# Kernel optimization log

Measured on AMD Instinct MI355X. Metric: run time of the kernel, lower is better.

Reference implementation:

```python
import jax, jax.numpy as jnp
import numpy as np
from jax import lax

N = 32768      # total nodes (8 graphs x 4096)
E = 262144     # edges (avg degree 8)
B = 8          # graphs in batch
TW = 25        # time window
H = 128        # hidden features
L = 6          # GNN layers
NV = 1         # n_variables (pos_t only)
SD = 1         # spatial dim
TMAX, TMIN, RES_T = 4.0, 0.0, 250.0
BD_LOW, BD_UP = 0.0, 16.0
EPS = 1e-5


def swish(x):
    return x * jax.nn.sigmoid(x)


def setup_inputs() -> dict:
    key = jax.random.key(0)
    ks = jax.random.split(key, 32)
    s = 0.05
    u = jax.random.normal(ks[0], (N, TW), jnp.float32)
    pos_t = jax.random.uniform(ks[1], (N, 1), jnp.float32) * TMAX
    pos_x = jax.random.uniform(ks[2], (N, 1), jnp.float32) * BD_UP
    pos = jnp.concatenate([pos_t, pos_x], axis=-1)
    edge_index = jax.random.randint(ks[3], (2, E), 0, N, jnp.int64)
    batch = jnp.repeat(jnp.arange(B, dtype=jnp.int64), N // B)
    d_in = TW + SD + NV          # 27
    d_msg = 2 * H + TW + SD + NV  # 282
    d_upd = H + H + NV            # 257
    We1 = jax.random.normal(ks[4], (d_in, H), jnp.float32) * s
    be1 = jnp.zeros((H,), jnp.float32)
    We2 = jax.random.normal(ks[5], (H, H), jnp.float32) * s
    be2 = jnp.zeros((H,), jnp.float32)
    Wm1 = jax.random.normal(ks[6], (L, d_msg, H), jnp.float32) * s
    bm1 = jnp.zeros((L, H), jnp.float32)
    Wm2 = jax.random.normal(ks[7], (L, H, H), jnp.float32) * s
    bm2 = jnp.zeros((L, H), jnp.float32)
    Wu1 = jax.random.normal(ks[8], (L, d_upd, H), jnp.float32) * s
    bu1 = jnp.zeros((L, H), jnp.float32)
    Wu2 = jax.random.normal(ks[9], (L, H, H), jnp.float32) * s
    bu2 = jnp.zeros((L, H), jnp.float32)
    Wc1 = jax.random.normal(ks[10], (8, 1, 16), jnp.float32) * s  # OIH
    bc1 = jnp.zeros((8,), jnp.float32)
    Wc2 = jax.random.normal(ks[11], (1, 8, 14), jnp.float32) * s
    bc2 = jnp.zeros((1,), jnp.float32)
    return dict(u=u, pos=pos, edge_index=edge_index, batch=batch,
                We1=We1, be1=be1, We2=We2, be2=be2,
                Wm1=Wm1, bm1=bm1, Wm2=Wm2, bm2=bm2,
                Wu1=Wu1, bu1=bu1, Wu2=Wu2, bu2=bu2,
                Wc1=Wc1, bc1=bc1, Wc2=Wc2, bc2=bc2)


def _mpnn(u, pos, edge_index, batch, We1, be1, We2, be2,
          Wm1, bm1, Wm2, bm2, Wu1, bu1, Wu2, bu2, Wc1, bc1, Wc2, bc2):
    src = edge_index[0]   # j (source)
    tgt = edge_index[1]   # i (target)
    pos_t = pos[:, 0:1] / TMAX
    pos_x = (pos[:, 1:] - BD_LOW) / (BD_UP - BD_LOW)
    variables = pos_t  # eq_variables empty -> only normalized time

    node_input = jnp.concatenate([u, pos_x, variables], axis=-1)  # [N, 27]
    h = swish(node_input @ We1 + be1)
    h = swish(h @ We2 + be2)

    # in-degree for scatter-mean (empty targets -> 0 like PyG mean)
    cnt = jnp.zeros((N,), jnp.float32).at[tgt].add(1.0)
    cnt = jnp.maximum(cnt, 1.0)[:, None]
    # per-graph node counts for InstanceNorm
    gcnt = jax.ops.segment_sum(jnp.ones((N,), jnp.float32), batch, num_segments=B)[:, None]

    u_diff_e = u[tgt] - u[src]          # [E, TW]
    p_diff_e = pos_x[tgt] - pos_x[src]  # [E, SD]
    var_i_e = variables[tgt]            # [E, NV]

    for l in range(L):
        # message: gather -> MLP per edge
        m_in = jnp.concatenate([h[tgt], h[src], u_diff_e, p_diff_e, var_i_e], axis=-1)  # [E, 282]
        msg = swish(m_in @ Wm1[l] + bm1[l])
        msg = swish(msg @ Wm2[l] + bm2[l])
        # scatter-mean aggregate onto targets
        agg = jax.ops.segment_sum(msg, tgt, num_segments=N) / cnt  # [N, H]
        # node update MLP, residual (in_features == out_features)
        up = jnp.concatenate([h, agg, variables], axis=-1)  # [N, 257]
        up = swish(up @ Wu1[l] + bu1[l])
        up = swish(up @ Wu2[l] + bu2[l])
        h = h + up
        # InstanceNorm per graph (no affine), biased variance
        mean = jax.ops.segment_sum(h, batch, num_segments=B) / gcnt      # [B, H]
        sq = jax.ops.segment_sum(h * h, batch, num_segments=B) / gcnt    # [B, H]
        var = sq - mean * mean
        h = (h - mean[batch]) / jnp.sqrt(var[batch] + EPS)

    # output CNN: tw=25 branch
    hc = h[:, None, :]  # [N, 1, 128]
    dn = ('NCH', 'OIH', 'NCH')
    c = lax.conv_general_dilated(hc, Wc1, (3,), 'VALID', dimension_numbers=dn) + bc1[None, :, None]
    c = swish(c)
    c = lax.conv_general_dilated(c, Wc2, (1,), 'VALID', dimension_numbers=dn) + bc2[None, :, None]
    diff = c[:, 0, :]  # [N, 25]

    dt = (TMAX - TMIN) / RES_T
    dt_cum = jnp.arange(1, TW + 1, dtype=jnp.float32) * dt  # cumsum of ones*dt
    out = u[:, -1:] + dt_cum[None, :] * diff
    return out


def reference(u, pos, edge_index, batch, We1, be1, We2, be2,
              Wm1, bm1, Wm2, bm2, Wu1, bu1, Wu2, bu2, Wc1, bc1, Wc2, bc2):
    return _mpnn(u, pos, edge_index, batch, We1, be1, We2, be2,
                 Wm1, bm1, Wm2, bm2, Wu1, bu1, Wu2, bu2, Wc1, bc1, Wc2, bc2)
```

## Files before the change

### kernel.cpp

```cpp
#include <hip/hip_runtime.h>
#include <stdint.h>

#define N_NODES 32768
#define N_EDGES 262144
#define NB 8
#define TW 25

typedef __attribute__((ext_vector_type(8))) short short8;
typedef __attribute__((ext_vector_type(4))) float floatx4;

#if defined(__has_builtin)
#if __has_builtin(__builtin_amdgcn_cvt_pk_bf16_f32)
#define HAVE_CVT_PK_BF16 1
#endif
#endif

__device__ __forceinline__ float swishf(float x) {
    return x * __builtin_amdgcn_rcpf(1.0f + __expf(-x));
}

__device__ __forceinline__ unsigned short f2bf(float x) {
    union { float f; unsigned u; } v; v.f = x;
    unsigned r = v.u + 0x7FFFu + ((v.u >> 16) & 1u);
    return (unsigned short)(r >> 16);
}
__device__ __forceinline__ unsigned pkbf(float a, float b) {
#ifdef HAVE_CVT_PK_BF16
    typedef __attribute__((ext_vector_type(2))) __bf16 bf16x2;
    union { bf16x2 v; unsigned u; } cv;
    cv.v = __builtin_amdgcn_cvt_pk_bf16_f32(a, b);
    return cv.u;
#else
    return (unsigned)f2bf(a) | ((unsigned)f2bf(b) << 16);
#endif
}
__device__ __forceinline__ float bf2f(unsigned short b) {
    union { unsigned u; float f; } v; v.u = ((unsigned)b) << 16; return v.f;
}

__global__ void init_kernel(const float* __restrict__ pos,
                            float* __restrict__ posx, float* __restrict__ post) {
    int i = blockIdx.x * 256 + threadIdx.x;
    if (i < N_NODES) {
        post[i] = pos[i * 2 + 0] * 0.25f;
        posx[i] = pos[i * 2 + 1] * 0.0625f;
    }
}

__global__ void deg_kernel(const int* __restrict__ tgt, int* __restrict__ deg) {
    int i = blockIdx.x * 256 + threadIdx.x;
    if (i < N_EDGES) atomicAdd(&deg[tgt[i]], 1);
}

__global__ __launch_bounds__(1024) void scan_kernel(const int* __restrict__ deg,
                                                    int* __restrict__ cursor) {
    __shared__ int ps[1024];
    int t = threadIdx.x;
    int base = t * 32;
    int tot = 0;
    for (int i = 0; i < 32; ++i) tot += deg[base + i];
    ps[t] = tot;
    __syncthreads();
    for (int off = 1; off < 1024; off <<= 1) {
        int v = (t >= off) ? ps[t - off] : 0;
        __syncthreads();
        ps[t] += v;
        __syncthreads();
    }
    int run = ps[t] - tot;
    for (int i = 0; i < 32; ++i) {
        cursor[base + i] = run;
        run += deg[base + i];
    }
}

__global__ void scatter_kernel(const int* __restrict__ src, const int* __restrict__ tgt,
                               int* __restrict__ cursor,
                               int* __restrict__ src_s, int* __restrict__ tgt_s) {
    int i = blockIdx.x * 256 + threadIdx.x;
    if (i < N_EDGES) {
        int tg = tgt[i];
        int p = atomicAdd(&cursor[tg], 1);
        src_s[p] = src[i];
        tgt_s[p] = tg;
    }
}

__global__ __launch_bounds__(256) void ediff_kernel(
    const float* __restrict__ u, const float* __restrict__ posx,
    const float* __restrict__ post,
    const int* __restrict__ src_s, const int* __restrict__ tgt_s,
    unsigned short* __restrict__ ediff)
{
    int e = blockIdx.x * 256 + threadIdx.x;
    if (e >= N_EDGES) return;
    int s = src_s[e], g = tgt_s[e];
    float fv[32];
    #pragma unroll
    for (int k = 0; k < 32; ++k) fv[k] = 0.f;
    #pragma unroll
    for (int k = 0; k < 25; ++k)
        fv[k] = u[(size_t)g * 25 + k] - u[(size_t)s * 25 + k];
    fv[25] = posx[g] - posx[s];
    fv[26] = post[g];
    unsigned pk[16];
    #pragma unroll
    for (int j = 0; j < 16; ++j) pk[j] = pkbf(fv[2 * j], fv[2 * j + 1]);
    #pragma unroll
    for (int j = 0; j < 4; ++j)
        *(uint4*)(ediff + (size_t)e * 32 + j * 8) = *(uint4*)&pk[j * 4];
}

__global__ __launch_bounds__(256) void pack_kernel(const float* __restrict__ W,
                                                   unsigned short* __restrict__ Wp,
                                                   int Kreal, int Kc, int total) {
    int id = blockIdx.x * 256 + threadIdx.x;
    if (id >= total) return;
    int lane = id & 63;
    int t8 = (id >> 6) & 7;
    int rest = id >> 9;
    int c = rest % Kc;
    int l = rest / Kc;
    int n = t8 * 16 + (lane & 15);
    int kb = c * 32 + (lane >> 4) * 8;
    short8 v;
    #pragma unroll
    for (int j = 0; j < 8; ++j) {
        int k = kb + j;
        float x = (k < Kreal) ? W[((size_t)l * Kreal + k) * 128 + n] : 0.f;
        v[j] = (short)f2bf(x);
    }
    *(short8*)(Wp + (size_t)id * 8) = v;
}

__global__ __launch_bounds__(256) void encoder_kernel(
    const float* __restrict__ u, const float* __restrict__ posx,
    const float* __restrict__ post,
    const float* __restrict__ We1, const float* __restrict__ be1,
    const float* __restrict__ We2, const float* __restrict__ be2,
    unsigned short* __restrict__ h_bf, float* __restrict__ agg)
{
    __shared__ __align__(16) float As[64 * 36];
    __shared__ __align__(16) float Ws[32 * 128];
    __shared__ __align__(16) float Ms[64 * 128];

    int t = threadIdx.x;
    int n0 = blockIdx.x * 64;
    int rg = t >> 5, cg = t & 31;

    {
        int r = t & 63, cseg = t >> 6;
        float4 z = make_float4(0.f, 0.f, 0.f, 0.f);
        #pragma unroll
        for (int j = 0; j < 8; ++j)
            *(float4*)(agg + (size_t)(n0 + r) * 128 + cseg * 32 + j * 4) = z;
    }

    float acc[8][4] = {};
    {
        int kk = t >> 3, cb = (t & 7) * 16;
        #pragma unroll
        for (int j = 0; j < 4; ++j) {
            float4 w = make_float4(0.f, 0.f, 0.f, 0.f);
            if (kk < 27) w = *(const float4*)&We1[kk * 128 + cb + j * 4];
            *(float4*)&Ws[kk * 128 + cb + j * 4] = w;
        }
        int el = t >> 2, kb = (t & 3) * 8, n = n0 + el;
        float v[8];
        #pragma unroll
        for (int j = 0; j < 8; ++j) {
            int k = kb + j;
            float x = 0.f;
            if (k < 25) x = u[n * 25 + k];
            else if (k == 25) x = posx[n];
            else if (k == 26) x = post[n];
            v[j] = x;
        }
        #pragma unroll
        for (int j = 0; j < 8; j += 4)
            *(float4*)&As[el * 36 + kb + j] = make_float4(v[j], v[j+1], v[j+2], v[j+3]);
        __syncthreads();
        #pragma unroll 4
        for (int kk2 = 0; kk2 < 32; ++kk2) {
            float4 b = *(const float4*)&Ws[kk2 * 128 + cg * 4];
            float a[8];
            #pragma unroll
            for (int i = 0; i < 8; ++i) a[i] = As[(rg * 8 + i) * 36 + kk2];
            #pragma unroll
            for (int i = 0; i < 8; ++i) {
                acc[i][0] += a[i] * b.x; acc[i][1] += a[i] * b.y;
                acc[i][2] += a[i] * b.z; acc[i][3] += a[i] * b.w;
            }
        }
        __syncthreads();
    }
    {
        float4 b1 = *(const float4*)&be1[cg * 4];
        #pragma unroll
        for (int i = 0; i < 8; ++i) {
            float4 m;
            m.x = swishf(acc[i][0] + b1.x);
            m.y = swishf(acc[i][1] + b1.y);
            m.z = swishf(acc[i][2] + b1.z);
            m.w = swishf(acc[i][3] + b1.w);
            *(float4*)&Ms[(rg * 8 + i) * 128 + cg * 4] = m;
        }
        __syncthreads();
    }
    float acc2[8][4] = {};
    for (int k0 = 0; k0 < 128; k0 += 32) {
        int kk = t >> 3, cb = (t & 7) * 16;
        #pragma unroll
        for (int j = 0; j < 4; ++j)
            *(float4*)&Ws[kk * 128 + cb + j * 4] =
                *(const float4*)&We2[(k0 + kk) * 128 + cb + j * 4];
        __syncthreads();
        #pragma unroll 4
        for (int kk2 = 0; kk2 < 32; ++kk2) {
            float4 b = *(const float4*)&Ws[kk2 * 128 + cg * 4];
            float a[8];
            #pragma unroll
            for (int i = 0; i < 8; ++i) a[i] = Ms[(rg * 8 + i) * 128 + (k0 + kk2)];
            #pragma unroll
            for (int i = 0; i < 8; ++i) {
                acc2[i][0] += a[i] * b.x; acc2[i][1] += a[i] * b.y;
                acc2[i][2] += a[i] * b.z; acc2[i][3] += a[i] * b.w;
            }
        }
        __syncthreads();
    }
    {
        float4 b2 = *(const float4*)&be2[cg * 4];
        #pragma unroll
        for (int i = 0; i < 8; ++i) {
            int n = n0 + rg * 8 + i;
            float4 o;
            o.x = swishf(acc2[i][0] + b2.x);
            o.y = swishf(acc2[i][1] + b2.y);
            o.z = swishf(acc2[i][2] + b2.z);
            o.w = swishf(acc2[i][3] + b2.w);
            uint2 pk;
            pk.x = pkbf(o.x, o.y);
            pk.y = pkbf(o.z, o.w);
            *(uint2*)(h_bf + (size_t)n * 128 + cg * 4) = pk;
        }
    }
}

__global__ __launch_bounds__(512, 8) void message_kernel(
    const unsigned short* __restrict__ h_bf,
    const unsigned short* __restrict__ ediff,
    const int* __restrict__ src_s, const int* __restrict__ tgt_s,
    const unsigned short* __restrict__ W1p, const float* __restrict__ b1,
    const unsigned short* __restrict__ W2p, const float* __restrict__ b2,
    float* __restrict__ agg, float* __restrict__ stats)
{
    __shared__ __align__(16) unsigned short SH[64 * 296];
    __shared__ int tgtS[64];
    unsigned short* Msh = SH;
    unsigned short* Cs  = SH + 9216;

    int t = threadIdx.x;
    int e0 = blockIdx.x * 64;
    if (blockIdx.x == 0 && t < 256) {
        float4 z = make_float4(0.f, 0.f, 0.f, 0.f);
        *(float4*)&stats[t * 8] = z;
        *(float4*)&stats[t * 8 + 4] = z;
    }
    if (t < 64) tgtS[t] = tgt_s[e0 + t];

    {
        int r = t & 63, cseg = t >> 6;
        int g = tgt_s[e0 + r], s = src_s[e0 + r];
        const short8* hg = (const short8*)(h_bf + (size_t)g * 128);
        const short8* hs = (const short8*)(h_bf + (size_t)s * 128);
        #pragma unroll
        for (int j = 0; j < 2; ++j) {
            int chunk = cseg * 2 + j;
            *(short8*)(SH + r * 296 + chunk * 8)       = hg[chunk];
            *(short8*)(SH + r * 296 + 128 + chunk * 8) = hs[chunk];
        }
        if (cseg < 4)
            *(short8*)(SH + r * 296 + 256 + cseg * 8) =
                *(const short8*)(ediff + (size_t)(e0 + r) * 32 + cseg * 8);
    }
    __syncthreads();

    int w = t >> 6, lane = t & 63, q = lane >> 4, m = lane & 15;

    floatx4 acc[4] = {};
    #pragma unroll
    for (int c = 0; c < 9; ++c) {
        short8 b = *(const short8*)(W1p + ((size_t)(c * 8 + w) * 64 + lane) * 8);
        #pragma unroll
        for (int g2 = 0; g2 < 4; ++g2) {
            short8 a = *(const short8*)(SH + (g2 * 16 + m) * 296 + c * 32 + q * 8);
            acc[g2] = __builtin_amdgcn_mfma_f32_16x16x32_bf16(a, b, acc[g2], 0, 0, 0);
        }
    }
    __syncthreads();

    {
        int col = w * 16 + m;
        float bv = b1[col];
        #pragma unroll
        for (int g2 = 0; g2 < 4; ++g2) {
            unsigned p01 = pkbf(swishf(acc[g2][0] + bv), swishf(acc[g2][1] + bv));
            unsigned p23 = pkbf(swishf(acc[g2][2] + bv), swishf(acc[g2][3] + bv));
            int base = g2 * 16 + q * 4;
            Msh[(base + 0) * 136 + col] = (unsigned short)p01;
            Msh[(base + 1) * 136 + col] = (unsigned short)(p01 >> 16);
            Msh[(base + 2) * 136 + col] = (unsigned short)p23;
            Msh[(base + 3) * 136 + col] = (unsigned short)(p23 >> 16);
        }
    }
    __syncthreads();

    floatx4 acc2[4] = {};
    #pragma unroll
    for (int c = 0; c < 4; ++c) {
        short8 b = *(const short8*)(W2p + ((size_t)(c * 8 + w) * 64 + lane) * 8);
        #pragma unroll
        for (int g2 = 0; g2 < 4; ++g2) {
            short8 a = *(const short8*)(Msh + (g2 * 16 + m) * 136 + c * 32 + q * 8);
            acc2[g2] = __builtin_amdgcn_mfma_f32_16x16x32_bf16(a, b, acc2[g2], 0, 0, 0);
        }
    }
    {
        int col = w * 16 + m;
        float bv = b2[col];
        #pragma unroll
        for (int g2 = 0; g2 < 4; ++g2) {
            unsigned p01 = pkbf(swishf(acc2[g2][0] + bv), swishf(acc2[g2][1] + bv));
            unsigned p23 = pkbf(swishf(acc2[g2][2] + bv), swishf(acc2[g2][3] + bv));
            int base = g2 * 16 + q * 4;
            Cs[(base + 0) * 132 + col] = (unsigned short)p01;
            Cs[(base + 1) * 132 + col] = (unsigned short)(p01 >> 16);
            Cs[(base + 2) * 132 + col] = (unsigned short)p23;
            Cs[(base + 3) * 132 + col] = (unsigned short)(p23 >> 16);
        }
    }
    __syncthreads();

    {
        int col = t & 127, seg = t >> 7;
        int r0 = seg * 16;
        float run = 0.f;
        int prev = tgtS[r0];
        bool atStart = true;
        #pragma unroll 4
        for (int i = 0; i < 16; ++i) {
            int tg = tgtS[r0 + i];
            if (tg != prev) {
                float* dst = &agg[(size_t)prev * 128 + col];
                if (atStart) atomicAdd(dst, run);
                else *dst = run;
                run = 0.f; prev = tg; atStart = false;
            }
            run += bf2f(Cs[(r0 + i) * 132 + col]);
        }
        atomicAdd(&agg[(size_t)prev * 128 + col], run);
    }
}

__global__ __launch_bounds__(512, 4) void update_kernel(
    unsigned short* __restrict__ hraw, const unsigned short* __restrict__ h_bf,
    float* __restrict__ agg, const int* __restrict__ deg,
    const float* __restrict__ post,
    const unsigned short* __restrict__ W1p, const float* __restrict__ b1,
    const unsigned short* __restrict__ W2p, const float* __restrict__ b2,
    float* __restrict__ stats)
{
    __shared__ __align__(16) unsigned short SH[64 * 296 + 64 * 136];
    unsigned short* Msh = SH + 64 * 296;

    int t = threadIdx.x;
    int n0 = blockIdx.x * 64;

    {
        int r = t & 63, cseg = t >> 6;
        int n = n0 + r;
        const short8* hn = (const short8*)(h_bf + (size_t)n * 128);
        #pragma unroll
        for (int j = 0; j < 2; ++j) {
            int chunk = cseg * 2 + j;
            *(short8*)(SH + r * 296 + chunk * 8) = hn[chunk];
        }
        float ic = __builtin_amdgcn_rcpf(fmaxf((float)deg[n], 1.0f));
        #pragma unroll
        for (int j = 0; j < 2; ++j) {
            int unit = cseg * 2 + j;
            const float* ap = agg + (size_t)n * 128 + unit * 8;
            float4 v0 = *(const float4*)ap;
            float4 v1 = *(const float4*)(ap + 4);
            unsigned pa[4];
            pa[0] = pkbf(v0.x * ic, v0.y * ic);
            pa[1] = pkbf(v0.z * ic, v0.w * ic);
            pa[2] = pkbf(v1.x * ic, v1.y * ic);
            pa[3] = pkbf(v1.z * ic, v1.w * ic);
            *(uint4*)(SH + r * 296 + 128 + unit * 8) = *(uint4*)pa;
        }
        if (cseg < 4) {
            short8 z;
            #pragma unroll
            for (int k = 0; k < 8; ++k) z[k] = 0;
            if (cseg == 0) z[0] = (short)f2bf(post[n]);
            *(short8*)(SH + r * 296 + 256 + cseg * 8) = z;
        }
    }
    __syncthreads();

    int w = t >> 6, lane = t & 63, q = lane >> 4, m = lane & 15;

    floatx4 acc[4] = {};
    #pragma unroll
    for (int c = 0; c < 9; ++c) {
        short8 b = *(const short8*)(W1p + ((size_t)(c * 8 + w) * 64 + lane) * 8);
        #pragma unroll
        for (int g2 = 0; g2 < 4; ++g2) {
            short8 a = *(const short8*)(SH + (g2 * 16 + m) * 296 + c * 32 + q * 8);
            acc[g2] = __builtin_amdgcn_mfma_f32_16x16x32_bf16(a, b, acc[g2], 0, 0, 0);
        }
    }
    {
        int col = w * 16 + m;
        float bv = b1[col];
        #pragma unroll
        for (int g2 = 0; g2 < 4; ++g2) {
            unsigned p01 = pkbf(swishf(acc[g2][0] + bv), swishf(acc[g2][1] + bv));
            unsigned p23 = pkbf(swishf(acc[g2][2] + bv), swishf(acc[g2][3] + bv));
            int base = g2 * 16 + q * 4;
            Msh[(base + 0) * 136 + col] = (unsigned short)p01;
            Msh[(base + 1) * 136 + col] = (unsigned short)(p01 >> 16);
            Msh[(base + 2) * 136 + col] = (unsigned short)p23;
            Msh[(base + 3) * 136 + col] = (unsigned short)(p23 >> 16);
        }
    }
    __syncthreads();

    floatx4 acc2[4] = {};
    #pragma unroll
    for (int c = 0; c < 4; ++c) {
        short8 b = *(const short8*)(W2p + ((size_t)(c * 8 + w) * 64 + lane) * 8);
        #pragma unroll
        for (int g2 = 0; g2 < 4; ++g2) {
            short8 a = *(const short8*)(Msh + (g2 * 16 + m) * 136 + c * 32 + q * 8);
            acc2[g2] = __builtin_amdgcn_mfma_f32_16x16x32_bf16(a, b, acc2[g2], 0, 0, 0);
        }
    }

    int bidx = n0 >> 12;
    int col = w * 16 + m;
    float bv = b2[col];
    float s = 0.f, s2 = 0.f;
    #pragma unroll
    for (int g2 = 0; g2 < 4; ++g2) {
        #pragma unroll
        for (int r = 0; r < 4; ++r) {
            int row = g2 * 16 + q * 4 + r;
            float res = bf2f(SH[row * 296 + col]);
            float hv = res + swishf(acc2[g2][r] + bv);
            hraw[(size_t)(n0 + row) * 128 + col] = f2bf(hv);
            s += hv; s2 += hv * hv;
        }
    }
    s  += __shfl_xor(s, 16);  s  += __shfl_xor(s, 32);
    s2 += __shfl_xor(s2, 16); s2 += __shfl_xor(s2, 32);
    if (q == 0) {
        atomicAdd(&stats[bidx * 128 + col], s);
        atomicAdd(&stats[(NB + bidx) * 128 + col], s2);
    }
    {
        int r = t & 63, cseg = t >> 6;
        float4 z = make_float4(0.f, 0.f, 0.f, 0.f);
        #pragma unroll
        for (int j = 0; j < 4; ++j)
            *(float4*)(agg + (size_t)(n0 + r) * 128 + cseg * 16 + j * 4) = z;
    }
}

__global__ __launch_bounds__(256) void norm_kernel(
    const unsigned short* __restrict__ hraw,
    unsigned short* __restrict__ h_bf,
    const float* __restrict__ stats)
{
    size_t id = (size_t)blockIdx.x * 256 + threadIdx.x;
    int n = (int)(id >> 5), c4 = (int)(id & 31) * 4;
    int b = n >> 12;
    float4 mn = *(const float4*)&stats[b * 128 + c4];
    float4 sq = *(const float4*)&stats[(NB + b) * 128 + c4];
    uint2 rawp = *(const uint2*)(hraw + (size_t)n * 128 + c4);
    float v0 = bf2f((unsigned short)(rawp.x & 0xffffu));
    float v1 = bf2f((unsigned short)(rawp.x >> 16));
    float v2 = bf2f((unsigned short)(rawp.y & 0xffffu));
    float v3 = bf2f((unsigned short)(rawp.y >> 16));
    float m0 = mn.x * (1.f / 4096.f), m1 = mn.y * (1.f / 4096.f);
    float m2 = mn.z * (1.f / 4096.f), m3 = mn.w * (1.f / 4096.f);
    float r0 = (v0 - m0) * rsqrtf(sq.x * (1.f / 4096.f) - m0 * m0 + 1e-5f);
    float r1 = (v1 - m1) * rsqrtf(sq.y * (1.f / 4096.f) - m1 * m1 + 1e-5f);
    float r2 = (v2 - m2) * rsqrtf(sq.z * (1.f / 4096.f) - m2 * m2 + 1e-5f);
    float r3 = (v3 - m3) * rsqrtf(sq.w * (1.f / 4096.f) - m3 * m3 + 1e-5f);
    uint2 pk;
    pk.x = pkbf(r0, r1);
    pk.y = pkbf(r2, r3);
    *(uint2*)(h_bf + (size_t)n * 128 + c4) = pk;
}

__global__ __launch_bounds__(256) void conv_kernel(
    const unsigned short* __restrict__ h_bf, const float* __restrict__ u,
    const float* __restrict__ Wc1, const float* __restrict__ bc1,
    const float* __restrict__ Wc2, const float* __restrict__ bc2,
    float* __restrict__ out)
{
    __shared__ float hs[4][128];
    __shared__ float c1[4][8 * 40];
    int w = threadIdx.x >> 6, lane = threadIdx.x & 63;
    int n = blockIdx.x * 4 + w;
    hs[w][lane]      = bf2f(h_bf[(size_t)n * 128 + lane]);
    hs[w][lane + 64] = bf2f(h_bf[(size_t)n * 128 + lane + 64]);
    __syncthreads();
    for (int idx = lane; idx < 304; idx += 64) {
        int o = idx / 38, p = idx % 38;
        float s = bc1[o];
        #pragma unroll
        for (int k = 0; k < 16; ++k) s += hs[w][p * 3 + k] * Wc1[o * 16 + k];
        c1[w][o * 40 + p] = swishf(s);
    }
    __syncthreads();
    if (lane < TW) {
        float s = bc2[0];
        #pragma unroll
        for (int o = 0; o < 8; ++o)
            for (int k = 0; k < 14; ++k)
                s += c1[w][o * 40 + lane + k] * Wc2[o * 14 + k];
        float dt_cum = (float)(lane + 1) * (4.0f / 250.0f);
        out[n * TW + lane] = u[n * 25 + 24] + dt_cum * s;
    }
}

extern "C" void kernel_launch(void* const* d_in, const int* in_sizes, int n_in,
                              void* d_out, int out_size, void* d_ws, size_t ws_size,
                              hipStream_t stream)
{
    const float* u   = (const float*)d_in[0];
    const float* pos = (const float*)d_in[1];
    const int*   ei  = (const int*)d_in[2];
    const float* We1 = (const float*)d_in[4];
    const float* be1 = (const float*)d_in[5];
    const float* We2 = (const float*)d_in[6];
    const float* be2 = (const float*)d_in[7];
    const float* Wm1 = (const float*)d_in[8];
    const float* bm1 = (const float*)d_in[9];
    const float* Wm2 = (const float*)d_in[10];
    const float* bm2 = (const float*)d_in[11];
    const float* Wu1 = (const float*)d_in[12];
    const float* bu1 = (const float*)d_in[13];
    const float* Wu2 = (const float*)d_in[14];
    const float* bu2 = (const float*)d_in[15];
    const float* Wc1 = (const float*)d_in[16];
    const float* bc1 = (const float*)d_in[17];
    const float* Wc2 = (const float*)d_in[18];
    const float* bc2 = (const float*)d_in[19];
    float* out = (float*)d_out;

    char* base = (char*)d_ws;
    size_t off = 0;
    auto alloc = [&](size_t bytes) -> char* {
        char* r = base + off;
        off = (off + bytes + 511) & ~(size_t)511;
        return r;
    };
    unsigned short* hraw   = (unsigned short*)alloc((size_t)N_NODES * 128 * 2);
    unsigned short* h_bf   = (unsigned short*)alloc((size_t)N_NODES * 128 * 2);
    float*          agg    = (float*)alloc((size_t)N_NODES * 128 * 4);
    float*          posx   = (float*)alloc(N_NODES * 4);
    float*          post   = (float*)alloc(N_NODES * 4);
    float*          stats  = (float*)alloc(2 * NB * 128 * 4);
    int*            deg    = (int*)alloc(N_NODES * 4);
    int*            cursor = (int*)alloc(N_NODES * 4);
    int*            src_s  = (int*)alloc((size_t)N_EDGES * 4);
    int*            tgt_s  = (int*)alloc((size_t)N_EDGES * 4);
    unsigned short* ediff  = (unsigned short*)alloc((size_t)N_EDGES * 32 * 2);
    unsigned short* Wm1p   = (unsigned short*)alloc((size_t)6 * 9 * 4096 * 2);
    unsigned short* Wm2p   = (unsigned short*)alloc((size_t)6 * 4 * 4096 * 2);
    unsigned short* Wu1p   = (unsigned short*)alloc((size_t)6 * 9 * 4096 * 2);
    unsigned short* Wu2p   = (unsigned short*)alloc((size_t)6 * 4 * 4096 * 2);
    (void)ws_size;

    const int* srcp = ei;
    const int* tgtp = ei + N_EDGES;

    init_kernel<<<N_NODES / 256, 256, 0, stream>>>(pos, posx, post);
    hipMemsetAsync(deg, 0, N_NODES * sizeof(int), stream);
    deg_kernel<<<N_EDGES / 256, 256, 0, stream>>>(tgtp, deg);
    scan_kernel<<<1, 1024, 0, stream>>>(deg, cursor);
    scatter_kernel<<<N_EDGES / 256, 256, 0, stream>>>(srcp, tgtp, cursor, src_s, tgt_s);
    ediff_kernel<<<N_EDGES / 256, 256, 0, stream>>>(u, posx, post, src_s, tgt_s, ediff);
    encoder_kernel<<<N_NODES / 64, 256, 0, stream>>>(u, posx, post, We1, be1, We2, be2,
                                                     h_bf, agg);
    {
        int tot1 = 6 * 9 * 512;
        int tot2 = 6 * 4 * 512;
        pack_kernel<<<(tot1 + 255) / 256, 256, 0, stream>>>(Wm1, Wm1p, 283, 9, tot1);
        pack_kernel<<<(tot2 + 255) / 256, 256, 0, stream>>>(Wm2, Wm2p, 128, 4, tot2);
        pack_kernel<<<(tot1 + 255) / 256, 256, 0, stream>>>(Wu1, Wu1p, 257, 9, tot1);
        pack_kernel<<<(tot2 + 255) / 256, 256, 0, stream>>>(Wu2, Wu2p, 128, 4, tot2);
    }

    for (int l = 0; l < 6; ++l) {
        message_kernel<<<N_EDGES / 64, 512, 0, stream>>>(
            h_bf, ediff, src_s, tgt_s,
            Wm1p + (size_t)l * 9 * 4096, bm1 + l * 128,
            Wm2p + (size_t)l * 4 * 4096, bm2 + l * 128, agg, stats);
        update_kernel<<<N_NODES / 64, 512, 0, stream>>>(
            hraw, h_bf, agg, deg, post,
            Wu1p + (size_t)l * 9 * 4096, bu1 + l * 128,
            Wu2p + (size_t)l * 4 * 4096, bu2 + l * 128, stats);
        norm_kernel<<<(N_NODES * 32) / 256, 256, 0, stream>>>(hraw, h_bf, stats);
    }

    conv_kernel<<<N_NODES / 4, 256, 0, stream>>>(h_bf, u, Wc1, bc1, Wc2, bc2, out);
}
```

Before: 676.8 us.

## Factor first message layer into per-node projections and fuse norm into premsg

Splits the first message-MLP linear layer by linearity: since its input is [h_i, h_j, u_i-u_j, x_i-x_j, t_i], it becomes a target-side projection and a source-side projection computed once per node. The edge kernel then only gathers two fp32 rows, adds them and applies swish before the second layer. This removes the per-edge 282x128 GEMM and the ediff buffer. Instance normalization is folded into the new per-node kernel and the conv kernel, so the separate norm pass goes away. The trade-off is larger fp32 gathers per edge (two 512-byte rows instead of bf16 rows) plus an extra node-level kernel each layer.

```diff
diff --git a/kernel.cpp b/kernel.cpp
--- a/kernel.cpp
+++ b/kernel.cpp
@@ -38,12 +38,25 @@
     union { unsigned u; float f; } v; v.u = ((unsigned)b) << 16; return v.f;
 }
 
-__global__ void init_kernel(const float* __restrict__ pos,
-                            float* __restrict__ posx, float* __restrict__ post) {
+__global__ void init_kernel(const float* __restrict__ pos, const float* __restrict__ u,
+                            float* __restrict__ posx, float* __restrict__ post,
+                            unsigned short* __restrict__ feat) {
     int i = blockIdx.x * 256 + threadIdx.x;
     if (i < N_NODES) {
-        post[i] = pos[i * 2 + 0] * 0.25f;
-        posx[i] = pos[i * 2 + 1] * 0.0625f;
+        float pt = pos[i * 2 + 0] * 0.25f;
+        float px = pos[i * 2 + 1] * 0.0625f;
+        post[i] = pt;
+        posx[i] = px;
+        unsigned short f[32];
+        #pragma unroll
+        for (int k = 0; k < 25; ++k) f[k] = f2bf(u[(size_t)i * 25 + k]);
+        f[25] = f2bf(px);
+        f[26] = f2bf(pt);
+        #pragma unroll
+        for (int k = 27; k < 32; ++k) f[k] = 0;
+        #pragma unroll
+        for (int j = 0; j < 4; ++j)
+            *(uint4*)(feat + (size_t)i * 32 + j * 8) = *(uint4*)&f[j * 8];
     }
 }
 
@@ -84,31 +97,6 @@
         src_s[p] = src[i];
         tgt_s[p] = tg;
     }
-}
-
-__global__ __launch_bounds__(256) void ediff_kernel(
-    const float* __restrict__ u, const float* __restrict__ posx,
-    const float* __restrict__ post,
-    const int* __restrict__ src_s, const int* __restrict__ tgt_s,
-    unsigned short* __restrict__ ediff)
-{
-    int e = blockIdx.x * 256 + threadIdx.x;
-    if (e >= N_EDGES) return;
-    int s = src_s[e], g = tgt_s[e];
-    float fv[32];
-    #pragma unroll
-    for (int k = 0; k < 32; ++k) fv[k] = 0.f;
-    #pragma unroll
-    for (int k = 0; k < 25; ++k)
-        fv[k] = u[(size_t)g * 25 + k] - u[(size_t)s * 25 + k];
-    fv[25] = posx[g] - posx[s];
-    fv[26] = post[g];
-    unsigned pk[16];
-    #pragma unroll
-    for (int j = 0; j < 16; ++j) pk[j] = pkbf(fv[2 * j], fv[2 * j + 1]);
-    #pragma unroll
-    for (int j = 0; j < 4; ++j)
-        *(uint4*)(ediff + (size_t)e * 32 + j * 8) = *(uint4*)&pk[j * 4];
 }
 
 __global__ __launch_bounds__(256) void pack_kernel(const float* __restrict__ W,
@@ -133,14 +121,45 @@
     *(short8*)(Wp + (size_t)id * 8) = v;
 }
 
+__global__ __launch_bounds__(256) void pack_cat_kernel(const float* __restrict__ Wm1,
+                                                       unsigned short* __restrict__ Wp) {
+    int id = blockIdx.x * 256 + threadIdx.x;
+    if (id >= 30720) return;
+    int lane = id & 63;
+    int tile = (id >> 6) & 15;
+    int rest = id >> 10;
+    int c = rest % 5;
+    int l = rest / 5;
+    int n = tile * 16 + (lane & 15);
+    int col = n & 127;
+    bool isT = n < 128;
+    int kb = c * 32 + (lane >> 4) * 8;
+    const float* W = Wm1 + (size_t)l * 283 * 128;
+    short8 v;
+    #pragma unroll
+    for (int j = 0; j < 8; ++j) {
+        int k = kb + j;
+        float x = 0.f;
+        if (k < 128) {
+            x = W[(size_t)(isT ? k : 128 + k) * 128 + col];
+        } else if (k < 155) {
+            int row = 256 + (k - 128);
+            x = W[(size_t)row * 128 + col];
+            if (!isT) x = (row == 282) ? 0.f : -x;
+        }
+        v[j] = (short)f2bf(x);
+    }
+    *(short8*)(Wp + (size_t)id * 8) = v;
+}
+
 __global__ __launch_bounds__(256) void encoder_kernel(
     const float* __restrict__ u, const float* __restrict__ posx,
     const float* __restrict__ post,
     const float* __restrict__ We1, const float* __restrict__ be1,
     const float* __restrict__ We2, const float* __restrict__ be2,
-    unsigned short* __restrict__ h_bf, float* __restrict__ agg)
+    unsigned short* __restrict__ hraw, float* __restrict__ agg)
 {
-    __shared__ __align__(16) float As[64 * 36];
+    __shared__ __align__(16) float As_[64 * 36];
     __shared__ __align__(16) float Ws[32 * 128];
     __shared__ __align__(16) float Ms[64 * 128];
 
@@ -178,14 +197,14 @@
         }
         #pragma unroll
         for (int j = 0; j < 8; j += 4)
-            *(float4*)&As[el * 36 + kb + j] = make_float4(v[j], v[j+1], v[j+2], v[j+3]);
+            *(float4*)&As_[el * 36 + kb + j] = make_float4(v[j], v[j+1], v[j+2], v[j+3]);
         __syncthreads();
         #pragma unroll 4
         for (int kk2 = 0; kk2 < 32; ++kk2) {
             float4 b = *(const float4*)&Ws[kk2 * 128 + cg * 4];
             float a[8];
             #pragma unroll
-            for (int i = 0; i < 8; ++i) a[i] = As[(rg * 8 + i) * 36 + kk2];
+            for (int i = 0; i < 8; ++i) a[i] = As_[(rg * 8 + i) * 36 + kk2];
             #pragma unroll
             for (int i = 0; i < 8; ++i) {
                 acc[i][0] += a[i] * b.x; acc[i][1] += a[i] * b.y;
@@ -242,23 +261,104 @@
             uint2 pk;
             pk.x = pkbf(o.x, o.y);
             pk.y = pkbf(o.z, o.w);
-            *(uint2*)(h_bf + (size_t)n * 128 + cg * 4) = pk;
+            *(uint2*)(hraw + (size_t)n * 128 + cg * 4) = pk;
+        }
+    }
+}
+
+__global__ __launch_bounds__(512, 4) void premsg_kernel(
+    const unsigned short* __restrict__ hraw,
+    const float* __restrict__ stats, int donorm,
+    const unsigned short* __restrict__ feat,
+    const unsigned short* __restrict__ Wp, const float* __restrict__ b1,
+    unsigned short* __restrict__ h_bf,
+    float* __restrict__ At, float* __restrict__ As)
+{
+    __shared__ __align__(16) unsigned short A[64 * 168];
+    __shared__ float mean_s[128];
+    __shared__ float rstd_s[128];
+
+    int t = threadIdx.x;
+    int n0 = blockIdx.x * 64;
+    int bidx = n0 >> 12;
+
+    if (t < 128) {
+        float mn = 0.f, rs = 1.f;
+        if (donorm) {
+            float s1 = stats[bidx * 128 + t] * (1.f / 4096.f);
+            float s2 = stats[(NB + bidx) * 128 + t] * (1.f / 4096.f);
+            mn = s1;
+            rs = rsqrtf(s2 - s1 * s1 + 1e-5f);
+        }
+        mean_s[t] = mn;
+        rstd_s[t] = rs;
+    }
+    __syncthreads();
+
+    {
+        int r = t & 63, cseg = t >> 6;
+        int n = n0 + r;
+        uint4 raw0 = *(const uint4*)(hraw + (size_t)n * 128 + cseg * 16);
+        uint4 raw1 = *(const uint4*)(hraw + (size_t)n * 128 + cseg * 16 + 8);
+        unsigned pk[8];
+        #pragma unroll
+        for (int j = 0; j < 8; ++j) {
+            unsigned word = (j < 4) ? ((const unsigned*)&raw0)[j]
+                                    : ((const unsigned*)&raw1)[j - 4];
+            int c0 = cseg * 16 + j * 2;
+            float v0 = (bf2f((unsigned short)(word & 0xffffu)) - mean_s[c0]) * rstd_s[c0];
+            float v1 = (bf2f((unsigned short)(word >> 16)) - mean_s[c0 + 1]) * rstd_s[c0 + 1];
+            pk[j] = pkbf(v0, v1);
+        }
+        *(uint4*)(A + r * 168 + cseg * 16)     = *(uint4*)&pk[0];
+        *(uint4*)(A + r * 168 + cseg * 16 + 8) = *(uint4*)&pk[4];
+        *(uint4*)(h_bf + (size_t)n * 128 + cseg * 16)     = *(uint4*)&pk[0];
+        *(uint4*)(h_bf + (size_t)n * 128 + cseg * 16 + 8) = *(uint4*)&pk[4];
+        if (cseg < 2) {
+            uint4 f0 = *(const uint4*)(feat + (size_t)n * 32 + cseg * 16);
+            uint4 f1 = *(const uint4*)(feat + (size_t)n * 32 + cseg * 16 + 8);
+            *(uint4*)(A + r * 168 + 128 + cseg * 16)     = f0;
+            *(uint4*)(A + r * 168 + 128 + cseg * 16 + 8) = f1;
+        }
+    }
+    __syncthreads();
+
+    int w = t >> 6, lane = t & 63, q = lane >> 4, m = lane & 15;
+    floatx4 accT[4] = {};
+    floatx4 accS[4] = {};
+    #pragma unroll
+    for (int c = 0; c < 5; ++c) {
+        short8 bT = *(const short8*)(Wp + ((size_t)(c * 16 + w) * 64 + lane) * 8);
+        short8 bS = *(const short8*)(Wp + ((size_t)(c * 16 + 8 + w) * 64 + lane) * 8);
+        #pragma unroll
+        for (int g2 = 0; g2 < 4; ++g2) {
+            short8 a = *(const short8*)(A + (g2 * 16 + m) * 168 + c * 32 + q * 8);
+            accT[g2] = __builtin_amdgcn_mfma_f32_16x16x32_bf16(a, bT, accT[g2], 0, 0, 0);
+            accS[g2] = __builtin_amdgcn_mfma_f32_16x16x32_bf16(a, bS, accS[g2], 0, 0, 0);
+        }
+    }
+    int col = w * 16 + m;
+    float bv = b1[col];
+    #pragma unroll
+    for (int g2 = 0; g2 < 4; ++g2) {
+        #pragma unroll
+        for (int r = 0; r < 4; ++r) {
+            int row = g2 * 16 + q * 4 + r;
+            At[(size_t)(n0 + row) * 128 + col] = accT[g2][r] + bv;
+            As[(size_t)(n0 + row) * 128 + col] = accS[g2][r];
         }
     }
 }
 
 __global__ __launch_bounds__(512, 8) void message_kernel(
-    const unsigned short* __restrict__ h_bf,
-    const unsigned short* __restrict__ ediff,
+    const float* __restrict__ At, const float* __restrict__ As,
     const int* __restrict__ src_s, const int* __restrict__ tgt_s,
-    const unsigned short* __restrict__ W1p, const float* __restrict__ b1,
     const unsigned short* __restrict__ W2p, const float* __restrict__ b2,
     float* __restrict__ agg, float* __restrict__ stats)
 {
-    __shared__ __align__(16) unsigned short SH[64 * 296];
+    __shared__ __align__(16) unsigned short Msh[64 * 136];
+    __shared__ __align__(16) unsigned short Cs[64 * 132];
     __shared__ int tgtS[64];
-    unsigned short* Msh = SH;
-    unsigned short* Cs  = SH + 9216;
 
     int t = threadIdx.x;
     int e0 = blockIdx.x * 64;
@@ -272,49 +372,21 @@
     {
         int r = t & 63, cseg = t >> 6;
         int g = tgt_s[e0 + r], s = src_s[e0 + r];
-        const short8* hg = (const short8*)(h_bf + (size_t)g * 128);
-        const short8* hs = (const short8*)(h_bf + (size_t)s * 128);
-        #pragma unroll
-        for (int j = 0; j < 2; ++j) {
-            int chunk = cseg * 2 + j;
-            *(short8*)(SH + r * 296 + chunk * 8)       = hg[chunk];
-            *(short8*)(SH + r * 296 + 128 + chunk * 8) = hs[chunk];
-        }
-        if (cseg < 4)
-            *(short8*)(SH + r * 296 + 256 + cseg * 8) =
-                *(const short8*)(ediff + (size_t)(e0 + r) * 32 + cseg * 8);
+        const float4* at = (const float4*)(At + (size_t)g * 128 + cseg * 16);
+        const float4* as = (const float4*)(As + (size_t)s * 128 + cseg * 16);
+        unsigned pk[8];
+        #pragma unroll
+        for (int j = 0; j < 4; ++j) {
+            float4 a = at[j], bb = as[j];
+            pk[2 * j]     = pkbf(swishf(a.x + bb.x), swishf(a.y + bb.y));
+            pk[2 * j + 1] = pkbf(swishf(a.z + bb.z), swishf(a.w + bb.w));
+        }
+        *(uint4*)(Msh + r * 136 + cseg * 16)     = *(uint4*)&pk[0];
+        *(uint4*)(Msh + r * 136 + cseg * 16 + 8) = *(uint4*)&pk[4];
     }
     __syncthreads();
 
     int w = t >> 6, lane = t & 63, q = lane >> 4, m = lane & 15;
-
-    floatx4 acc[4] = {};
-    #pragma unroll
-    for (int c = 0; c < 9; ++c) {
-        short8 b = *(const short8*)(W1p + ((size_t)(c * 8 + w) * 64 + lane) * 8);
-        #pragma unroll
-        for (int g2 = 0; g2 < 4; ++g2) {
-            short8 a = *(const short8*)(SH + (g2 * 16 + m) * 296 + c * 32 + q * 8);
-            acc[g2] = __builtin_amdgcn_mfma_f32_16x16x32_bf16(a, b, acc[g2], 0, 0, 0);
-        }
-    }
-    __syncthreads();
-
-    {
-        int col = w * 16 + m;
-        float bv = b1[col];
-        #pragma unroll
-        for (int g2 = 0; g2 < 4; ++g2) {
-            unsigned p01 = pkbf(swishf(acc[g2][0] + bv), swishf(acc[g2][1] + bv));
-            unsigned p23 = pkbf(swishf(acc[g2][2] + bv), swishf(acc[g2][3] + bv));
-            int base = g2 * 16 + q * 4;
-            Msh[(base + 0) * 136 + col] = (unsigned short)p01;
-            Msh[(base + 1) * 136 + col] = (unsigned short)(p01 >> 16);
-            Msh[(base + 2) * 136 + col] = (unsigned short)p23;
-            Msh[(base + 3) * 136 + col] = (unsigned short)(p23 >> 16);
-        }
-    }
-    __syncthreads();
 
     floatx4 acc2[4] = {};
     #pragma unroll
@@ -479,35 +551,9 @@
     }
 }
 
-__global__ __launch_bounds__(256) void norm_kernel(
-    const unsigned short* __restrict__ hraw,
-    unsigned short* __restrict__ h_bf,
-    const float* __restrict__ stats)
-{
-    size_t id = (size_t)blockIdx.x * 256 + threadIdx.x;
-    int n = (int)(id >> 5), c4 = (int)(id & 31) * 4;
-    int b = n >> 12;
-    float4 mn = *(const float4*)&stats[b * 128 + c4];
-    float4 sq = *(const float4*)&stats[(NB + b) * 128 + c4];
-    uint2 rawp = *(const uint2*)(hraw + (size_t)n * 128 + c4);
-    float v0 = bf2f((unsigned short)(rawp.x & 0xffffu));
-    float v1 = bf2f((unsigned short)(rawp.x >> 16));
-    float v2 = bf2f((unsigned short)(rawp.y & 0xffffu));
-    float v3 = bf2f((unsigned short)(rawp.y >> 16));
-    float m0 = mn.x * (1.f / 4096.f), m1 = mn.y * (1.f / 4096.f);
-    float m2 = mn.z * (1.f / 4096.f), m3 = mn.w * (1.f / 4096.f);
-    float r0 = (v0 - m0) * rsqrtf(sq.x * (1.f / 4096.f) - m0 * m0 + 1e-5f);
-    float r1 = (v1 - m1) * rsqrtf(sq.y * (1.f / 4096.f) - m1 * m1 + 1e-5f);
-    float r2 = (v2 - m2) * rsqrtf(sq.z * (1.f / 4096.f) - m2 * m2 + 1e-5f);
-    float r3 = (v3 - m3) * rsqrtf(sq.w * (1.f / 4096.f) - m3 * m3 + 1e-5f);
-    uint2 pk;
-    pk.x = pkbf(r0, r1);
-    pk.y = pkbf(r2, r3);
-    *(uint2*)(h_bf + (size_t)n * 128 + c4) = pk;
-}
-
 __global__ __launch_bounds__(256) void conv_kernel(
-    const unsigned short* __restrict__ h_bf, const float* __restrict__ u,
+    const unsigned short* __restrict__ hraw, const float* __restrict__ stats,
+    const float* __restrict__ u,
     const float* __restrict__ Wc1, const float* __restrict__ bc1,
     const float* __restrict__ Wc2, const float* __restrict__ bc2,
     float* __restrict__ out)
@@ -516,8 +562,15 @@
     __shared__ float c1[4][8 * 40];
     int w = threadIdx.x >> 6, lane = threadIdx.x & 63;
     int n = blockIdx.x * 4 + w;
-    hs[w][lane]      = bf2f(h_bf[(size_t)n * 128 + lane]);
-    hs[w][lane + 64] = bf2f(h_bf[(size_t)n * 128 + lane + 64]);
+    int b = n >> 12;
+    #pragma unroll
+    for (int h2 = 0; h2 < 2; ++h2) {
+        int c = lane + h2 * 64;
+        float s1 = stats[b * 128 + c] * (1.f / 4096.f);
+        float s2 = stats[(NB + b) * 128 + c] * (1.f / 4096.f);
+        float rs = rsqrtf(s2 - s1 * s1 + 1e-5f);
+        hs[w][c] = (bf2f(hraw[(size_t)n * 128 + c]) - s1) * rs;
+    }
     __syncthreads();
     for (int idx = lane; idx < 304; idx += 64) {
         int o = idx / 38, p = idx % 38;
@@ -573,15 +626,17 @@
     unsigned short* hraw   = (unsigned short*)alloc((size_t)N_NODES * 128 * 2);
     unsigned short* h_bf   = (unsigned short*)alloc((size_t)N_NODES * 128 * 2);
     float*          agg    = (float*)alloc((size_t)N_NODES * 128 * 4);
+    float*          At     = (float*)alloc((size_t)N_NODES * 128 * 4);
+    float*          As     = (float*)alloc((size_t)N_NODES * 128 * 4);
     float*          posx   = (float*)alloc(N_NODES * 4);
     float*          post   = (float*)alloc(N_NODES * 4);
+    unsigned short* feat   = (unsigned short*)alloc((size_t)N_NODES * 32 * 2);
     float*          stats  = (float*)alloc(2 * NB * 128 * 4);
     int*            deg    = (int*)alloc(N_NODES * 4);
     int*            cursor = (int*)alloc(N_NODES * 4);
     int*            src_s  = (int*)alloc((size_t)N_EDGES * 4);
     int*            tgt_s  = (int*)alloc((size_t)N_EDGES * 4);
-    unsigned short* ediff  = (unsigned short*)alloc((size_t)N_EDGES * 32 * 2);
-    unsigned short* Wm1p   = (unsigned short*)alloc((size_t)6 * 9 * 4096 * 2);
+    unsigned short* Wcat1p = (unsigned short*)alloc((size_t)6 * 5 * 16 * 64 * 8 * 2);
     unsigned short* Wm2p   = (unsigned short*)alloc((size_t)6 * 4 * 4096 * 2);
     unsigned short* Wu1p   = (unsigned short*)alloc((size_t)6 * 9 * 4096 * 2);
     unsigned short* Wu2p   = (unsigned short*)alloc((size_t)6 * 4 * 4096 * 2);
@@ -590,34 +645,35 @@
     const int* srcp = ei;
     const int* tgtp = ei + N_EDGES;
 
-    init_kernel<<<N_NODES / 256, 256, 0, stream>>>(pos, posx, post);
+    init_kernel<<<N_NODES / 256, 256, 0, stream>>>(pos, u, posx, post, feat);
     hipMemsetAsync(deg, 0, N_NODES * sizeof(int), stream);
     deg_kernel<<<N_EDGES / 256, 256, 0, stream>>>(tgtp, deg);
     scan_kernel<<<1, 1024, 0, stream>>>(deg, cursor);
     scatter_kernel<<<N_EDGES / 256, 256, 0, stream>>>(srcp, tgtp, cursor, src_s, tgt_s);
-    ediff_kernel<<<N_EDGES / 256, 256, 0, stream>>>(u, posx, post, src_s, tgt_s, ediff);
     encoder_kernel<<<N_NODES / 64, 256, 0, stream>>>(u, posx, post, We1, be1, We2, be2,
-                                                     h_bf, agg);
-    {
+                                                     hraw, agg);
+    {
+        pack_cat_kernel<<<120, 256, 0, stream>>>(Wm1, Wcat1p);
         int tot1 = 6 * 9 * 512;
         int tot2 = 6 * 4 * 512;
-        pack_kernel<<<(tot1 + 255) / 256, 256, 0, stream>>>(Wm1, Wm1p, 283, 9, tot1);
         pack_kernel<<<(tot2 + 255) / 256, 256, 0, stream>>>(Wm2, Wm2p, 128, 4, tot2);
         pack_kernel<<<(tot1 + 255) / 256, 256, 0, stream>>>(Wu1, Wu1p, 257, 9, tot1);
         pack_kernel<<<(tot2 + 255) / 256, 256, 0, stream>>>(Wu2, Wu2p, 128, 4, tot2);
     }
 
     for (int l = 0; l < 6; ++l) {
+        premsg_kernel<<<N_NODES / 64, 512, 0, stream>>>(
+            hraw, stats, (l > 0) ? 1 : 0, feat,
+            Wcat1p + (size_t)l * 5 * 16 * 64 * 8, bm1 + l * 128,
+            h_bf, At, As);
         message_kernel<<<N_EDGES / 64, 512, 0, stream>>>(
-            h_bf, ediff, src_s, tgt_s,
-            Wm1p + (size_t)l * 9 * 4096, bm1 + l * 128,
+            At, As, src_s, tgt_s,
             Wm2p + (size_t)l * 4 * 4096, bm2 + l * 128, agg, stats);
         update_kernel<<<N_NODES / 64, 512, 0, stream>>>(
             hraw, h_bf, agg, deg, post,
             Wu1p + (size_t)l * 9 * 4096, bu1 + l * 128,
             Wu2p + (size_t)l * 4 * 4096, bu2 + l * 128, stats);
-        norm_kernel<<<(N_NODES * 32) / 256, 256, 0, stream>>>(hraw, h_bf, stats);
-    }
-
-    conv_kernel<<<N_NODES / 4, 256, 0, stream>>>(h_bf, u, Wc1, bc1, Wc2, bc2, out);
-}
+    }
+
+    conv_kernel<<<N_NODES / 4, 256, 0, stream>>>(hraw, stats, u, Wc1, bc1, Wc2, bc2, out);
+}
```

Measured after the change: 650.5 us. -3.9%, faster.
